# Performance work log

Measured on AMD Instinct MI355X. Metric: run time of the kernel, lower is better.

## Reference

```python
import jax, jax.numpy as jnp
import numpy as np

GENE_NUM = 3000
N_NODES = 50000
N_EDGES = 1000000
DIM = 128


def setup_inputs() -> dict:
    key = jax.random.key(0)
    ks = jax.random.split(key, 8)
    h = jax.random.normal(ks[0], (N_NODES, DIM), dtype=jnp.float32)
    alpha = jax.random.normal(ks[1], (GENE_NUM + 2,), dtype=jnp.float32)
    edge_weight = jax.random.uniform(ks[2], (N_EDGES,), dtype=jnp.float32)
    # Xavier-uniform Linear weight, zero bias
    gain = float(np.sqrt(2.0))  # calculate_gain('relu')
    bound = gain * np.sqrt(6.0 / (DIM + DIM))
    W = jax.random.uniform(ks[3], (DIM, DIM), minval=-bound, maxval=bound, dtype=jnp.float32)
    b = jnp.zeros((DIM,), dtype=jnp.float32)
    # node ids: genes 0..GENE_NUM-1 have id = gene index (>=0); cells have id = -1 (<0)
    node_id = jnp.concatenate([
        jnp.arange(GENE_NUM, dtype=jnp.int64),
        -jnp.ones((N_NODES - GENE_NUM,), dtype=jnp.int64),
    ])
    edge_src = jax.random.randint(ks[4], (N_EDGES,), 0, N_NODES, dtype=jnp.int64)
    edge_dst = jax.random.randint(ks[5], (N_EDGES,), 0, N_NODES, dtype=jnp.int64)
    return {"h": h, "alpha": alpha, "edge_weight": edge_weight, "W": W, "b": b,
            "node_id": node_id, "edge_src": edge_src, "edge_dst": edge_dst}


def reference(h, alpha, edge_weight, W, b, node_id, edge_src, edge_dst):
    gene_num = alpha.shape[0] - 2
    src_id = node_id[edge_src]  # [E]
    dst_id = node_id[edge_dst]  # [E]
    # default: cell self-loop alpha -> index gene_num + 1
    idx = jnp.full(edge_src.shape, gene_num + 1, dtype=jnp.int32)
    idx = jnp.where((src_id >= 0) & (dst_id < 0), src_id.astype(jnp.int32), idx)   # gene->cell: beta[src]
    idx = jnp.where((dst_id >= 0) & (src_id < 0), dst_id.astype(jnp.int32), idx)   # cell->gene: beta[dst]
    idx = jnp.where((dst_id >= 0) & (src_id >= 0), gene_num, idx)                  # gene self-loop alpha
    # gather -> per-edge message [E, D]
    coeff = alpha[idx] * edge_weight                     # [E]
    msg = h[edge_src] * coeff[:, None]                   # [E, D]
    # scatter-mean over destination nodes
    n = h.shape[0]
    summ = jax.ops.segment_sum(msg, edge_dst, num_segments=n)           # [N, D]
    cnt = jax.ops.segment_sum(jnp.ones_like(edge_weight), edge_dst, num_segments=n)
    neigh = summ / jnp.maximum(cnt, 1.0)[:, None]
    # MLP: dropout(eval, identity) -> Linear -> ReLU -> norm(identity)
    z = jax.nn.relu(neigh @ W.T + b)
    return z
```

## Files before the change

kernel.cpp:

```cpp
#include <hip/hip_runtime.h>

#define D 128
#define PSHIFT 7
#define PSIZE 128
#define EDGES_PER_BLK 4096
#define CAP 4608

typedef __attribute__((ext_vector_type(8))) short bf16x8;
typedef __attribute__((ext_vector_type(4))) float f32x4;

__device__ __forceinline__ unsigned short f2bf(float f) {
  unsigned int u = __float_as_uint(f);
  u = (u + 0x7fffu + ((u >> 16) & 1)) >> 16;
  return (unsigned short)u;
}

__global__ __launch_bounds__(256) void cvt_kernel(
    const float* __restrict__ h, unsigned short* __restrict__ h16, int total4) {
  int i = blockIdx.x * blockDim.x + threadIdx.x;
  if (i >= total4) return;
  float4 v = ((const float4*)h)[i];
  ushort4 o;
  o.x = f2bf(v.x); o.y = f2bf(v.y); o.z = f2bf(v.z); o.w = f2bf(v.w);
  ((ushort4*)h16)[i] = o;
}

__global__ __launch_bounds__(512) void bin_hist_kernel(
    const int* __restrict__ edst, int* __restrict__ g_hist, int E) {
  __shared__ int cnt[512];
  int t = threadIdx.x;
  cnt[t] = 0;
  __syncthreads();
  int eb = blockIdx.x * EDGES_PER_BLK;
#pragma unroll
  for (int q = 0; q < 8; ++q) {
    int e = eb + q * 512 + t;
    if (e < E) atomicAdd(&cnt[edst[e] >> PSHIFT], 1);
  }
  __syncthreads();
  int c = cnt[t];
  if (c > 0) atomicAdd(&g_hist[t], c);
}

__global__ __launch_bounds__(512) void part_scan_kernel(
    const int* __restrict__ g_hist, int* __restrict__ part_off,
    int* __restrict__ g_cursor, int E) {
  __shared__ int ts[512];
  int t = threadIdx.x;
  int v = g_hist[t];
  ts[t] = v;
  __syncthreads();
  for (int off = 1; off < 512; off <<= 1) {
    int x = (t >= off) ? ts[t - off] : 0;
    __syncthreads();
    ts[t] += x;
    __syncthreads();
  }
  int excl = ts[t] - v;
  part_off[t] = excl;
  g_cursor[t] = excl;
  if (t == 0) part_off[512] = E;
}

__global__ __launch_bounds__(512) void bin_scatter_kernel(
    const float* __restrict__ alpha, const float* __restrict__ ew,
    const int* __restrict__ node_id, const int* __restrict__ esrc,
    const int* __restrict__ edst, int* __restrict__ g_cursor,
    int2* __restrict__ recs, int E, int gene_num) {
  __shared__ int2 lrec[EDGES_PER_BLK];
  __shared__ unsigned short lbin[EDGES_PER_BLK];
  __shared__ int cnt[512], offl[512], gbase[512];

  int t = threadIdx.x;
  cnt[t] = 0;
  __syncthreads();

  int eb = blockIdx.x * EDGES_PER_BLK;
  int rx[8]; float rc[8]; int rb[8]; int rk[8];
#pragma unroll
  for (int q = 0; q < 8; ++q) {
    int e = eb + q * 512 + t;
    rk[q] = -1;
    if (e < E) {
      int src = esrc[e];
      int dst = edst[e];
      int sid = node_id[src];
      int did = node_id[dst];
      int idx;
      if (sid >= 0) idx = (did >= 0) ? gene_num : sid;
      else          idx = (did >= 0) ? did : (gene_num + 1);
      rc[q] = alpha[idx] * ew[e];
      rx[q] = src | ((dst & (PSIZE - 1)) << 16);
      int b = dst >> PSHIFT;
      rb[q] = b;
      rk[q] = atomicAdd(&cnt[b], 1);
    }
  }
  __syncthreads();

  {
    int v = cnt[t];
    offl[t] = v;
    __syncthreads();
    for (int off = 1; off < 512; off <<= 1) {
      int x = (t >= off) ? offl[t - off] : 0;
      __syncthreads();
      offl[t] += x;
      __syncthreads();
    }
    int incl = offl[t];
    __syncthreads();
    offl[t] = incl - v;
  }
  __syncthreads();

#pragma unroll
  for (int q = 0; q < 8; ++q) {
    if (rk[q] >= 0) {
      int ls = offl[rb[q]] + rk[q];
      lrec[ls] = make_int2(rx[q], __float_as_int(rc[q]));
      lbin[ls] = (unsigned short)rb[q];
    }
  }
  __syncthreads();

  {
    int c = cnt[t];
    if (c > 0) gbase[t] = atomicAdd(&g_cursor[t], c);
  }
  __syncthreads();

  int tot = E - eb;
  if (tot > EDGES_PER_BLK) tot = EDGES_PER_BLK;
  for (int s = t; s < tot; s += 512) {
    int b = lbin[s];
    recs[gbase[b] + (s - offl[b])] = lrec[s];
  }
}

__global__ __launch_bounds__(512) void part_acc_kernel(
    const unsigned short* __restrict__ h16, const int2* __restrict__ recs,
    const int* __restrict__ part_off, float* __restrict__ neigh, int N) {
  __shared__ int2 lrec[CAP];
  __shared__ unsigned short perm[CAP];
  __shared__ int cnt[PSIZE], offl[PSIZE];

  int t = threadIdx.x;
  int p = blockIdx.x;
  if (t < PSIZE) cnt[t] = 0;
  __syncthreads();

  int start = part_off[p];
  int R = part_off[p + 1] - start;
  if (R > CAP) R = CAP;

  int dlq[9]; int rkq[9];
#pragma unroll
  for (int q = 0; q < 9; ++q) {
    int s = q * 512 + t;
    rkq[q] = -1;
    if (s < R) {
      int2 r = recs[start + s];
      lrec[s] = r;
      int dl = (r.x >> 16) & (PSIZE - 1);
      dlq[q] = dl;
      rkq[q] = atomicAdd(&cnt[dl], 1);
    }
  }
  __syncthreads();

  {
    int v = 0;
    if (t < PSIZE) { v = cnt[t]; offl[t] = v; }
    __syncthreads();
    for (int off = 1; off < PSIZE; off <<= 1) {
      int x = 0;
      if (t < PSIZE && t >= off) x = offl[t - off];
      __syncthreads();
      if (t < PSIZE) offl[t] += x;
      __syncthreads();
    }
    if (t < PSIZE) {
      int incl = offl[t];
      offl[t] = incl - v;
    }
  }
  __syncthreads();

#pragma unroll
  for (int q = 0; q < 9; ++q) {
    if (rkq[q] >= 0) perm[offl[dlq[q]] + rkq[q]] = (unsigned short)(q * 512 + t);
  }
  __syncthreads();

  int w = t >> 6;
  int l = t & 63;
  const unsigned int* hp = ((const unsigned int*)h16) + l;

  for (int dd = 0; dd < 16; ++dd) {
    int dl = w * 16 + dd;
    int dst = p * PSIZE + dl;
    if (dst >= N) continue;
    int c = cnt[dl];
    int o = offl[dl];
    float ax = 0.f, ay = 0.f;
    for (int base = 0; base < c; base += 64) {
      int j = base + l;
      int2 r = make_int2(0, 0);
      if (j < c) r = lrec[perm[o + j]];
      int m = c - base;
      if (m > 64) m = 64;
      int k = 0;
      for (; k + 8 <= m; k += 8) {
        int ss[8]; float cc[8]; unsigned int vv[8];
#pragma unroll
        for (int q = 0; q < 8; ++q) {
          ss[q] = __shfl(r.x, k + q) & 0xffff;
          cc[q] = __int_as_float(__shfl(r.y, k + q));
        }
#pragma unroll
        for (int q = 0; q < 8; ++q) vv[q] = hp[(size_t)ss[q] * 64];
#pragma unroll
        for (int q = 0; q < 8; ++q) {
          ax += cc[q] * __uint_as_float(vv[q] << 16);
          ay += cc[q] * __uint_as_float(vv[q] & 0xffff0000u);
        }
      }
      for (; k + 4 <= m; k += 4) {
        int ss[4]; float cc[4]; unsigned int vv[4];
#pragma unroll
        for (int q = 0; q < 4; ++q) {
          ss[q] = __shfl(r.x, k + q) & 0xffff;
          cc[q] = __int_as_float(__shfl(r.y, k + q));
        }
#pragma unroll
        for (int q = 0; q < 4; ++q) vv[q] = hp[(size_t)ss[q] * 64];
#pragma unroll
        for (int q = 0; q < 4; ++q) {
          ax += cc[q] * __uint_as_float(vv[q] << 16);
          ay += cc[q] * __uint_as_float(vv[q] & 0xffff0000u);
        }
      }
      for (; k < m; ++k) {
        int sv = __shfl(r.x, k) & 0xffff;
        float cf = __int_as_float(__shfl(r.y, k));
        unsigned int v = hp[(size_t)sv * 64];
        ax += cf * __uint_as_float(v << 16);
        ay += cf * __uint_as_float(v & 0xffff0000u);
      }
    }
    float inv = 1.0f / (float)(c > 0 ? c : 1);
    ((float2*)neigh)[(size_t)dst * (D / 2) + l] = make_float2(ax * inv, ay * inv);
  }
}

__global__ __launch_bounds__(256) void mlp_mfma_kernel(
    const float* __restrict__ W, const float* __restrict__ bias,
    float* __restrict__ io, int N) {
  __shared__ __align__(16) unsigned short Wl[128 * 128];

  int t = threadIdx.x;
#pragma unroll
  for (int i = 0; i < 8; ++i) {
    int chunk = t + 256 * i;
    int row = chunk >> 4;
    int cb = chunk & 15;
    const float* gp = W + (size_t)row * 128 + cb * 8;
    float4 a = *(const float4*)gp;
    float4 b = *(const float4*)(gp + 4);
    bf16x8 v;
    v[0] = (short)f2bf(a.x); v[1] = (short)f2bf(a.y);
    v[2] = (short)f2bf(a.z); v[3] = (short)f2bf(a.w);
    v[4] = (short)f2bf(b.x); v[5] = (short)f2bf(b.y);
    v[6] = (short)f2bf(b.z); v[7] = (short)f2bf(b.w);
    *(bf16x8*)((char*)Wl + row * 256 + ((cb ^ (row & 7)) << 4)) = v;
  }
  __syncthreads();

  int l = t & 63;
  int w = t >> 6;
  int kg = l >> 4;
  int m_base = blockIdx.x * 64 + w * 16;
  int arow = m_base + (l & 15);
  if (arow >= N) arow = N - 1;

  bf16x8 af[4];
  const float* ap = io + (size_t)arow * 128 + kg * 8;
#pragma unroll
  for (int kk = 0; kk < 4; ++kk) {
    float4 a = *(const float4*)(ap + kk * 32);
    float4 b = *(const float4*)(ap + kk * 32 + 4);
    bf16x8 v;
    v[0] = (short)f2bf(a.x); v[1] = (short)f2bf(a.y);
    v[2] = (short)f2bf(a.z); v[3] = (short)f2bf(a.w);
    v[4] = (short)f2bf(b.x); v[5] = (short)f2bf(b.y);
    v[6] = (short)f2bf(b.z); v[7] = (short)f2bf(b.w);
    af[kk] = v;
  }

#pragma unroll
  for (int c = 0; c < 8; ++c) {
    f32x4 acc = {0.f, 0.f, 0.f, 0.f};
    int row_w = c * 16 + (l & 15);
    int rs = row_w & 7;
#pragma unroll
    for (int kk = 0; kk < 4; ++kk) {
      int cb = kk * 4 + kg;
      bf16x8 bf = *(bf16x8*)((char*)Wl + row_w * 256 + ((cb ^ rs) << 4));
      acc = __builtin_amdgcn_mfma_f32_16x16x32_bf16(af[kk], bf, acc, 0, 0, 0);
    }
    int j = c * 16 + (l & 15);
    float bj = bias[j];
#pragma unroll
    for (int r = 0; r < 4; ++r) {
      int m = m_base + kg * 4 + r;
      if (m < N) io[(size_t)m * 128 + j] = fmaxf(acc[r] + bj, 0.0f);
    }
  }
}

extern "C" void kernel_launch(void* const* d_in, const int* in_sizes, int n_in,
                              void* d_out, int out_size, void* d_ws, size_t ws_size,
                              hipStream_t stream) {
  const float* h     = (const float*)d_in[0];
  const float* alpha = (const float*)d_in[1];
  const float* ew    = (const float*)d_in[2];
  const float* W     = (const float*)d_in[3];
  const float* bias  = (const float*)d_in[4];
  const int* node_id = (const int*)d_in[5];
  const int* esrc    = (const int*)d_in[6];
  const int* edst    = (const int*)d_in[7];
  float* out = (float*)d_out;

  int E = in_sizes[2];
  int N = in_sizes[5];
  int gene_num = in_sizes[1] - 2;
  int npart = (N + PSIZE - 1) / PSIZE;
  int eblocks = (E + EDGES_PER_BLK - 1) / EDGES_PER_BLK;

  int* g_hist   = (int*)d_ws;
  int* part_off = g_hist + 512;
  int* g_cursor = part_off + 513;
  size_t h16_off = ((size_t)(512 + 513 + 512) * sizeof(int) + 15) & ~(size_t)15;
  unsigned short* h16 = (unsigned short*)((char*)d_ws + h16_off);
  size_t rec_off = (h16_off + (size_t)N * D * sizeof(unsigned short) + 15) & ~(size_t)15;
  int2* recs = (int2*)((char*)d_ws + rec_off);
  size_t need = rec_off + (size_t)E * sizeof(int2);
  if (ws_size < need) return;

  hipMemsetAsync(g_hist, 0, 512 * sizeof(int), stream);

  {
    int total4 = N * D / 4;
    cvt_kernel<<<(total4 + 255) / 256, 256, 0, stream>>>(h, h16, total4);
  }
  bin_hist_kernel<<<eblocks, 512, 0, stream>>>(edst, g_hist, E);
  part_scan_kernel<<<1, 512, 0, stream>>>(g_hist, part_off, g_cursor, E);
  bin_scatter_kernel<<<eblocks, 512, 0, stream>>>(alpha, ew, node_id, esrc,
                                                  edst, g_cursor, recs, E,
                                                  gene_num);
  part_acc_kernel<<<npart, 512, 0, stream>>>(h16, recs, part_off, out, N);
  {
    int blocks = (N + 63) / 64;
    mlp_mfma_kernel<<<blocks, 256, 0, stream>>>(W, bias, out, N);
  }
}
```

Baseline: 117.0 us.

## Halve destination partition size, fuse convert with histogram, drop perm indirection

Shrinks the destination partitions from 128 to 64 nodes, so there are about 782 partitions, with more accumulate blocks and smaller per-block LDS staging. Records are now held in registers and written straight into sorted LDS order, which removes the perm indirection array and one LDS read per edge. The bf16 conversion and the bin histogram are merged into a single launch, split by block index, which saves a kernel launch. The scans become two-per-thread to handle up to 1024 bins. The risks are overflow in partitions with more than 2048 edges (silently capped) and extra atomics traffic from doubling the bin count.

```diff
diff --git a/kernel.cpp b/kernel.cpp
--- a/kernel.cpp
+++ b/kernel.cpp
@@ -1,10 +1,11 @@
 #include <hip/hip_runtime.h>
 
 #define D 128
-#define PSHIFT 7
-#define PSIZE 128
+#define PSHIFT 6
+#define PSIZE 64
 #define EDGES_PER_BLK 4096
-#define CAP 4608
+#define CAP 2048
+#define MAXPART 1024
 
 typedef __attribute__((ext_vector_type(8))) short bf16x8;
 typedef __attribute__((ext_vector_type(4))) float f32x4;
@@ -15,23 +16,24 @@
   return (unsigned short)u;
 }
 
-__global__ __launch_bounds__(256) void cvt_kernel(
-    const float* __restrict__ h, unsigned short* __restrict__ h16, int total4) {
-  int i = blockIdx.x * blockDim.x + threadIdx.x;
-  if (i >= total4) return;
-  float4 v = ((const float4*)h)[i];
-  ushort4 o;
-  o.x = f2bf(v.x); o.y = f2bf(v.y); o.z = f2bf(v.z); o.w = f2bf(v.w);
-  ((ushort4*)h16)[i] = o;
-}
-
-__global__ __launch_bounds__(512) void bin_hist_kernel(
-    const int* __restrict__ edst, int* __restrict__ g_hist, int E) {
-  __shared__ int cnt[512];
-  int t = threadIdx.x;
-  cnt[t] = 0;
-  __syncthreads();
-  int eb = blockIdx.x * EDGES_PER_BLK;
+__global__ __launch_bounds__(512) void cvt_hist_kernel(
+    const float* __restrict__ h, unsigned short* __restrict__ h16, int total4,
+    const int* __restrict__ edst, int* __restrict__ g_hist, int E,
+    int cvtBlocks) {
+  if ((int)blockIdx.x < cvtBlocks) {
+    int i = blockIdx.x * 512 + threadIdx.x;
+    if (i >= total4) return;
+    float4 v = ((const float4*)h)[i];
+    ushort4 o;
+    o.x = f2bf(v.x); o.y = f2bf(v.y); o.z = f2bf(v.z); o.w = f2bf(v.w);
+    ((ushort4*)h16)[i] = o;
+    return;
+  }
+  __shared__ int cnt[MAXPART];
+  int t = threadIdx.x;
+  cnt[t] = 0; cnt[t + 512] = 0;
+  __syncthreads();
+  int eb = (blockIdx.x - cvtBlocks) * EDGES_PER_BLK;
 #pragma unroll
   for (int q = 0; q < 8; ++q) {
     int e = eb + q * 512 + t;
@@ -40,15 +42,19 @@
   __syncthreads();
   int c = cnt[t];
   if (c > 0) atomicAdd(&g_hist[t], c);
+  c = cnt[t + 512];
+  if (c > 0) atomicAdd(&g_hist[t + 512], c);
 }
 
 __global__ __launch_bounds__(512) void part_scan_kernel(
     const int* __restrict__ g_hist, int* __restrict__ part_off,
-    int* __restrict__ g_cursor, int E) {
+    int* __restrict__ g_cursor, int E, int npart) {
   __shared__ int ts[512];
   int t = threadIdx.x;
-  int v = g_hist[t];
-  ts[t] = v;
+  int i0 = 2 * t, i1 = 2 * t + 1;
+  int v0 = (i0 < npart) ? g_hist[i0] : 0;
+  int v1 = (i1 < npart) ? g_hist[i1] : 0;
+  ts[t] = v0 + v1;
   __syncthreads();
   for (int off = 1; off < 512; off <<= 1) {
     int x = (t >= off) ? ts[t - off] : 0;
@@ -56,10 +62,10 @@
     ts[t] += x;
     __syncthreads();
   }
-  int excl = ts[t] - v;
-  part_off[t] = excl;
-  g_cursor[t] = excl;
-  if (t == 0) part_off[512] = E;
+  int excl = ts[t] - (v0 + v1);
+  if (i0 < npart) { part_off[i0] = excl; g_cursor[i0] = excl; }
+  if (i1 < npart) { part_off[i1] = excl + v0; g_cursor[i1] = excl + v0; }
+  if (t == 0) part_off[npart] = E;
 }
 
 __global__ __launch_bounds__(512) void bin_scatter_kernel(
@@ -69,10 +75,11 @@
     int2* __restrict__ recs, int E, int gene_num) {
   __shared__ int2 lrec[EDGES_PER_BLK];
   __shared__ unsigned short lbin[EDGES_PER_BLK];
-  __shared__ int cnt[512], offl[512], gbase[512];
-
-  int t = threadIdx.x;
-  cnt[t] = 0;
+  __shared__ int cnt[MAXPART], offl[MAXPART], gbase[MAXPART];
+  __shared__ int ts[512];
+
+  int t = threadIdx.x;
+  cnt[t] = 0; cnt[t + 512] = 0;
   __syncthreads();
 
   int eb = blockIdx.x * EDGES_PER_BLK;
@@ -98,20 +105,18 @@
   }
   __syncthreads();
 
-  {
-    int v = cnt[t];
-    offl[t] = v;
-    __syncthreads();
-    for (int off = 1; off < 512; off <<= 1) {
-      int x = (t >= off) ? offl[t - off] : 0;
-      __syncthreads();
-      offl[t] += x;
-      __syncthreads();
-    }
-    int incl = offl[t];
-    __syncthreads();
-    offl[t] = incl - v;
-  }
+  int c0 = cnt[2 * t], c1 = cnt[2 * t + 1];
+  ts[t] = c0 + c1;
+  __syncthreads();
+  for (int off = 1; off < 512; off <<= 1) {
+    int x = (t >= off) ? ts[t - off] : 0;
+    __syncthreads();
+    ts[t] += x;
+    __syncthreads();
+  }
+  int exclp = ts[t] - (c0 + c1);
+  offl[2 * t] = exclp;
+  offl[2 * t + 1] = exclp + c0;
   __syncthreads();
 
 #pragma unroll
@@ -127,6 +132,8 @@
   {
     int c = cnt[t];
     if (c > 0) gbase[t] = atomicAdd(&g_cursor[t], c);
+    c = cnt[t + 512];
+    if (c > 0) gbase[t + 512] = atomicAdd(&g_cursor[t + 512], c);
   }
   __syncthreads();
 
@@ -142,7 +149,6 @@
     const unsigned short* __restrict__ h16, const int2* __restrict__ recs,
     const int* __restrict__ part_off, float* __restrict__ neigh, int N) {
   __shared__ int2 lrec[CAP];
-  __shared__ unsigned short perm[CAP];
   __shared__ int cnt[PSIZE], offl[PSIZE];
 
   int t = threadIdx.x;
@@ -154,14 +160,14 @@
   int R = part_off[p + 1] - start;
   if (R > CAP) R = CAP;
 
-  int dlq[9]; int rkq[9];
-#pragma unroll
-  for (int q = 0; q < 9; ++q) {
+  int2 rq[4]; int dlq[4]; int rkq[4];
+#pragma unroll
+  for (int q = 0; q < 4; ++q) {
     int s = q * 512 + t;
     rkq[q] = -1;
     if (s < R) {
       int2 r = recs[start + s];
-      lrec[s] = r;
+      rq[q] = r;
       int dl = (r.x >> 16) & (PSIZE - 1);
       dlq[q] = dl;
       rkq[q] = atomicAdd(&cnt[dl], 1);
@@ -169,36 +175,29 @@
   }
   __syncthreads();
 
-  {
-    int v = 0;
-    if (t < PSIZE) { v = cnt[t]; offl[t] = v; }
-    __syncthreads();
-    for (int off = 1; off < PSIZE; off <<= 1) {
-      int x = 0;
-      if (t < PSIZE && t >= off) x = offl[t - off];
-      __syncthreads();
-      if (t < PSIZE) offl[t] += x;
-      __syncthreads();
-    }
-    if (t < PSIZE) {
-      int incl = offl[t];
-      offl[t] = incl - v;
-    }
-  }
-  __syncthreads();
-
-#pragma unroll
-  for (int q = 0; q < 9; ++q) {
-    if (rkq[q] >= 0) perm[offl[dlq[q]] + rkq[q]] = (unsigned short)(q * 512 + t);
-  }
+  if (t < PSIZE) offl[t] = cnt[t];
+  __syncthreads();
+  for (int off = 1; off < PSIZE; off <<= 1) {
+    int x = 0;
+    if (t < PSIZE && t >= off) x = offl[t - off];
+    __syncthreads();
+    if (t < PSIZE) offl[t] += x;
+    __syncthreads();
+  }
+  if (t < PSIZE) offl[t] -= cnt[t];
+  __syncthreads();
+
+#pragma unroll
+  for (int q = 0; q < 4; ++q)
+    if (rkq[q] >= 0) lrec[offl[dlq[q]] + rkq[q]] = rq[q];
   __syncthreads();
 
   int w = t >> 6;
   int l = t & 63;
   const unsigned int* hp = ((const unsigned int*)h16) + l;
 
-  for (int dd = 0; dd < 16; ++dd) {
-    int dl = w * 16 + dd;
+  for (int dd = 0; dd < 8; ++dd) {
+    int dl = w * 8 + dd;
     int dst = p * PSIZE + dl;
     if (dst >= N) continue;
     int c = cnt[dl];
@@ -207,7 +206,7 @@
     for (int base = 0; base < c; base += 64) {
       int j = base + l;
       int2 r = make_int2(0, 0);
-      if (j < c) r = lrec[perm[o + j]];
+      if (j < c) r = lrec[o + j];
       int m = c - base;
       if (m > 64) m = 64;
       int k = 0;
@@ -337,25 +336,24 @@
   int gene_num = in_sizes[1] - 2;
   int npart = (N + PSIZE - 1) / PSIZE;
   int eblocks = (E + EDGES_PER_BLK - 1) / EDGES_PER_BLK;
+  int total4 = N * D / 4;
+  int cvtBlocks = (total4 + 511) / 512;
 
   int* g_hist   = (int*)d_ws;
-  int* part_off = g_hist + 512;
-  int* g_cursor = part_off + 513;
-  size_t h16_off = ((size_t)(512 + 513 + 512) * sizeof(int) + 15) & ~(size_t)15;
+  int* part_off = g_hist + MAXPART;
+  int* g_cursor = part_off + MAXPART + 1;
+  size_t h16_off = ((size_t)(3 * MAXPART + 1) * sizeof(int) + 15) & ~(size_t)15;
   unsigned short* h16 = (unsigned short*)((char*)d_ws + h16_off);
   size_t rec_off = (h16_off + (size_t)N * D * sizeof(unsigned short) + 15) & ~(size_t)15;
   int2* recs = (int2*)((char*)d_ws + rec_off);
   size_t need = rec_off + (size_t)E * sizeof(int2);
   if (ws_size < need) return;
 
-  hipMemsetAsync(g_hist, 0, 512 * sizeof(int), stream);
-
-  {
-    int total4 = N * D / 4;
-    cvt_kernel<<<(total4 + 255) / 256, 256, 0, stream>>>(h, h16, total4);
-  }
-  bin_hist_kernel<<<eblocks, 512, 0, stream>>>(edst, g_hist, E);
-  part_scan_kernel<<<1, 512, 0, stream>>>(g_hist, part_off, g_cursor, E);
+  hipMemsetAsync(g_hist, 0, MAXPART * sizeof(int), stream);
+
+  cvt_hist_kernel<<<cvtBlocks + eblocks, 512, 0, stream>>>(
+      h, h16, total4, edst, g_hist, E, cvtBlocks);
+  part_scan_kernel<<<1, 512, 0, stream>>>(g_hist, part_off, g_cursor, E, npart);
   bin_scatter_kernel<<<eblocks, 512, 0, stream>>>(alpha, ew, node_id, esrc,
                                                   edst, g_cursor, recs, E,
                                                   gene_num);
```

Result: faster. 113.6 us (-2.8%).
